# Kernel optimization log

Measured on AMD Instinct MI355X. Metric: run time of the kernel, lower is better.

The kernel has to match this reference:

```python
import jax, jax.numpy as jnp
import numpy as np

B, T, D = 8, 128, 1024   # batch, seq, n_embd
V, R, H = 4096, 16, 2    # vocab_size, rank, horizon


def setup_inputs() -> dict:
    key = jax.random.key(0)
    k1, k2, k3 = jax.random.split(key, 3)
    # scale 0.02 keeps exp(logits) numerically tame (pre-exp std ~ 0.6)
    last_hidden_state = jax.random.normal(k1, (B, T, D), jnp.float32) * 0.02
    param_w = jax.random.normal(k2, (V * R * H, D), jnp.float32) * 0.02
    param_b = jnp.zeros((V * R * H,), jnp.float32)
    points = jax.random.randint(k3, (B, H), 0, V, dtype=jnp.int64)
    return {
        "last_hidden_state": last_hidden_state,
        "param_w": param_w,
        "param_b": param_b,
        "points": points,
    }


def reference(last_hidden_state, param_w, param_b, points):
    # Take last timestep: (B, D)
    h_last = last_hidden_state[:, -1, :]
    # Linear + exp positivity: (B, H*V*R)
    params = jnp.exp(h_last @ param_w.T + param_b)
    # reshape to (B, H, V, R) matching torch .reshape(-1, horizon, vocab, rank)
    a = params.reshape(B, H, V, R)
    # CP outer product over rank: p_tilde[b,i,j] = sum_r a[b,0,i,r] * a[b,1,j,r]
    p_tilde = jnp.einsum('bir,bjr->bij', a[:, 0], a[:, 1])  # (B, V, V)
    # evaluate_at_points: gather p_tilde[b, points[b,0], points[b,1]]
    p_eval = p_tilde[jnp.arange(B), points[:, 0], points[:, 1]]  # (B,)
    # get_norm_const: sum over both vocab dims
    norm_const = p_tilde.sum(axis=(1, 2))  # (B,)
    return p_eval, norm_const
```

## Files before the change

### kernel.cpp

```cpp
#include <hip/hip_runtime.h>
#include <math.h>


#define B_ 8
#define T_ 128
#define D_ 1024
#define V_ 4096
#define R_ 16
#define H_ 2

__global__ void init_ws_kernel(float* ws) {
    int i = threadIdx.x;
    if (i < 512) ws[i] = 0.0f;
}

__device__ __forceinline__ float folded_reduce8(const float* p, int lane) {
    float t[4];
    {
        const bool hi = lane & 1;
#pragma unroll
        for (int i = 0; i < 4; ++i) {
            float send = hi ? p[i] : p[i + 4];
            float recv = __shfl_xor(send, 1);
            float keep = hi ? p[i + 4] : p[i];
            t[i] = keep + recv;
        }
    }
    float u[2];
    {
        const bool hi = lane & 2;
#pragma unroll
        for (int i = 0; i < 2; ++i) {
            float send = hi ? t[i] : t[i + 2];
            float recv = __shfl_xor(send, 2);
            float keep = hi ? t[i + 2] : t[i];
            u[i] = keep + recv;
        }
    }
    float wv;
    {
        const bool hi = lane & 4;
        float send = hi ? u[0] : u[1];
        float recv = __shfl_xor(send, 4);
        float keep = hi ? u[1] : u[0];
        wv = keep + recv;
    }
    wv += __shfl_xor(wv, 8);
    wv += __shfl_xor(wv, 16);
    wv += __shfl_xor(wv, 32);
    return wv;
}

__global__ __launch_bounds__(64, 2) void cpdist_main(
    const float* __restrict__ hid,
    const float* __restrict__ W,
    const float* __restrict__ bias,
    const int*   __restrict__ points,
    float* __restrict__ ws)
{
    const int lane = threadIdx.x;
    const int blk  = blockIdx.x;
    const int pair = blk >> 6;
    const int h    = pair >> 4;
    const int r    = pair & 15;
    const int v0   = (blk & 63) << 6;

    const int myb = ((lane & 1) << 2) | (lane & 2) | ((lane >> 2) & 1);

    float4 hreg[8][4];
#pragma unroll
    for (int b = 0; b < 8; ++b) {
        const float* hb = hid + ((size_t)b * T_ + (T_ - 1)) * D_;
#pragma unroll
        for (int j = 0; j < 4; ++j)
            hreg[b][j] = *reinterpret_cast<const float4*>(hb + j * 256 + lane * 4);
    }

    const int pv = points[myb * H_ + h];

    const size_t rowStride = (size_t)R_ * D_;
    const size_t row0 = ((size_t)h * V_ + v0) * R_ + r;
    const float* wp = W + row0 * D_;
    const float* bp = bias + row0;

    float4 cur[8];
#pragma unroll
    for (int j = 0; j < 4; ++j) {
        cur[j]     = *reinterpret_cast<const float4*>(wp + j * 256 + lane * 4);
        cur[4 + j] = *reinterpret_cast<const float4*>(wp + rowStride + j * 256 + lane * 4);
    }

    float accS = 0.0f;
    const int eidx = 256 + (myb * H_ + h) * R_ + r;

    for (int it = 0; it < 64; it += 2) {
        float4 nxt[8];
        if (it < 62) {
            const float* wn = wp + 2 * rowStride;
#pragma unroll
            for (int j = 0; j < 4; ++j) {
                nxt[j]     = *reinterpret_cast<const float4*>(wn + j * 256 + lane * 4);
                nxt[4 + j] = *reinterpret_cast<const float4*>(wn + rowStride + j * 256 + lane * 4);
            }
        }

        const float biasA = bp[(size_t)it * R_];
        const float biasB = bp[(size_t)(it + 1) * R_];

        float p[8];
#pragma unroll
        for (int b = 0; b < 8; ++b) {
            float s = 0.0f;
#pragma unroll
            for (int j = 0; j < 4; ++j) {
                s = fmaf(cur[j].x, hreg[b][j].x, s);
                s = fmaf(cur[j].y, hreg[b][j].y, s);
                s = fmaf(cur[j].z, hreg[b][j].z, s);
                s = fmaf(cur[j].w, hreg[b][j].w, s);
            }
            p[b] = s;
        }
        const float wvA = folded_reduce8(p, lane);

#pragma unroll
        for (int b = 0; b < 8; ++b) {
            float s = 0.0f;
#pragma unroll
            for (int j = 0; j < 4; ++j) {
                s = fmaf(cur[4 + j].x, hreg[b][j].x, s);
                s = fmaf(cur[4 + j].y, hreg[b][j].y, s);
                s = fmaf(cur[4 + j].z, hreg[b][j].z, s);
                s = fmaf(cur[4 + j].w, hreg[b][j].w, s);
            }
            p[b] = s;
        }
        const float wvB = folded_reduce8(p, lane);

        const float valA = __expf(wvA + biasA);
        const float valB = __expf(wvB + biasB);
        accS += valA;
        accS += valB;

        if (lane < 8) {
            if (v0 + it == pv)     ws[eidx] = valA;
            if (v0 + it + 1 == pv) ws[eidx] = valB;
        }

        if (it < 62) {
#pragma unroll
            for (int j = 0; j < 8; ++j) cur[j] = nxt[j];
            wp += 2 * rowStride;
        }
    }

    if (lane < 8)
        atomicAdd(&ws[(myb * H_ + h) * R_ + r], accS);
}

__global__ void cpdist_finalize(const float* __restrict__ ws, float* __restrict__ out) {
    const int tid = threadIdx.x;
    const int b = tid >> 4;
    const int r = tid & 15;
    const float e0 = ws[256 + (b * 2 + 0) * 16 + r];
    const float e1 = ws[256 + (b * 2 + 1) * 16 + r];
    const float s0 = ws[(b * 2 + 0) * 16 + r];
    const float s1 = ws[(b * 2 + 1) * 16 + r];
    float pe = e0 * e1;
    float nc = s0 * s1;
#pragma unroll
    for (int m = 1; m < 16; m <<= 1) {
        pe += __shfl_xor(pe, m);
        nc += __shfl_xor(nc, m);
    }
    if (r == 0) {
        out[b] = pe;
        out[8 + b] = nc;
    }
}

extern "C" void kernel_launch(void* const* d_in, const int* in_sizes, int n_in,
                              void* d_out, int out_size, void* d_ws, size_t ws_size,
                              hipStream_t stream) {
    const float* hid    = (const float*)d_in[0];
    const float* W      = (const float*)d_in[1];
    const float* bias   = (const float*)d_in[2];
    const int*   points = (const int*)d_in[3];
    float* out = (float*)d_out;
    float* ws  = (float*)d_ws;

    hipLaunchKernelGGL(init_ws_kernel, dim3(1), dim3(512), 0, stream, ws);
    hipLaunchKernelGGL(cpdist_main, dim3(2048), dim3(64), 0, stream,
                       hid, W, bias, points, ws);
    hipLaunchKernelGGL(cpdist_finalize, dim3(1), dim3(128), 0, stream, ws, out);
}
```

Before: 680.7 us.

## Replace atomic accumulation with per-block partial sums and stagger weight prefetch

Each block now writes its partial exp-sum to a dedicated workspace slot, and the finalize kernel reduces those partials. This removes the init kernel launch and the atomicAdd contention. The weight prefetch is also split so the next A rows load right after A is consumed and the next B rows load right after B is consumed, which replaces the full double buffer with a smaller staggered one and lowers register pressure. The finalize kernel does more serial work per thread, and the point-evaluation slots still rely on being written exactly once without being zeroed.

Result: no change. 671.7 us (-1.3%).

```diff
diff --git a/kernel.cpp b/kernel.cpp
--- a/kernel.cpp
+++ b/kernel.cpp
@@ -8,11 +8,6 @@
 #define V_ 4096
 #define R_ 16
 #define H_ 2
-
-__global__ void init_ws_kernel(float* ws) {
-    int i = threadIdx.x;
-    if (i < 512) ws[i] = 0.0f;
-}
 
 __device__ __forceinline__ float folded_reduce8(const float* p, int lane) {
     float t[4];
@@ -63,7 +58,8 @@
     const int pair = blk >> 6;
     const int h    = pair >> 4;
     const int r    = pair & 15;
-    const int v0   = (blk & 63) << 6;
+    const int vblk = blk & 63;
+    const int v0   = vblk << 6;
 
     const int myb = ((lane & 1) << 2) | (lane & 2) | ((lane >> 2) & 1);
 
@@ -83,27 +79,17 @@
     const float* wp = W + row0 * D_;
     const float* bp = bias + row0;
 
-    float4 cur[8];
+    float4 A[4], Bf[4];
 #pragma unroll
     for (int j = 0; j < 4; ++j) {
-        cur[j]     = *reinterpret_cast<const float4*>(wp + j * 256 + lane * 4);
-        cur[4 + j] = *reinterpret_cast<const float4*>(wp + rowStride + j * 256 + lane * 4);
+        A[j]  = *reinterpret_cast<const float4*>(wp + j * 256 + lane * 4);
+        Bf[j] = *reinterpret_cast<const float4*>(wp + rowStride + j * 256 + lane * 4);
     }
 
     float accS = 0.0f;
-    const int eidx = 256 + (myb * H_ + h) * R_ + r;
+    const int eidx = 16384 + (myb * H_ + h) * R_ + r;
 
     for (int it = 0; it < 64; it += 2) {
-        float4 nxt[8];
-        if (it < 62) {
-            const float* wn = wp + 2 * rowStride;
-#pragma unroll
-            for (int j = 0; j < 4; ++j) {
-                nxt[j]     = *reinterpret_cast<const float4*>(wn + j * 256 + lane * 4);
-                nxt[4 + j] = *reinterpret_cast<const float4*>(wn + rowStride + j * 256 + lane * 4);
-            }
-        }
-
         const float biasA = bp[(size_t)it * R_];
         const float biasB = bp[(size_t)(it + 1) * R_];
 
@@ -113,28 +99,42 @@
             float s = 0.0f;
 #pragma unroll
             for (int j = 0; j < 4; ++j) {
-                s = fmaf(cur[j].x, hreg[b][j].x, s);
-                s = fmaf(cur[j].y, hreg[b][j].y, s);
-                s = fmaf(cur[j].z, hreg[b][j].z, s);
-                s = fmaf(cur[j].w, hreg[b][j].w, s);
+                s = fmaf(A[j].x, hreg[b][j].x, s);
+                s = fmaf(A[j].y, hreg[b][j].y, s);
+                s = fmaf(A[j].z, hreg[b][j].z, s);
+                s = fmaf(A[j].w, hreg[b][j].w, s);
             }
             p[b] = s;
         }
         const float wvA = folded_reduce8(p, lane);
+
+        if (it < 62) {
+            const float* wn = wp + (size_t)(it + 2) * rowStride;
+#pragma unroll
+            for (int j = 0; j < 4; ++j)
+                A[j] = *reinterpret_cast<const float4*>(wn + j * 256 + lane * 4);
+        }
 
 #pragma unroll
         for (int b = 0; b < 8; ++b) {
             float s = 0.0f;
 #pragma unroll
             for (int j = 0; j < 4; ++j) {
-                s = fmaf(cur[4 + j].x, hreg[b][j].x, s);
-                s = fmaf(cur[4 + j].y, hreg[b][j].y, s);
-                s = fmaf(cur[4 + j].z, hreg[b][j].z, s);
-                s = fmaf(cur[4 + j].w, hreg[b][j].w, s);
+                s = fmaf(Bf[j].x, hreg[b][j].x, s);
+                s = fmaf(Bf[j].y, hreg[b][j].y, s);
+                s = fmaf(Bf[j].z, hreg[b][j].z, s);
+                s = fmaf(Bf[j].w, hreg[b][j].w, s);
             }
             p[b] = s;
         }
         const float wvB = folded_reduce8(p, lane);
+
+        if (it < 62) {
+            const float* wn = wp + (size_t)(it + 3) * rowStride;
+#pragma unroll
+            for (int j = 0; j < 4; ++j)
+                Bf[j] = *reinterpret_cast<const float4*>(wn + j * 256 + lane * 4);
+        }
 
         const float valA = __expf(wvA + biasA);
         const float valB = __expf(wvB + biasB);
@@ -145,34 +145,38 @@
             if (v0 + it == pv)     ws[eidx] = valA;
             if (v0 + it + 1 == pv) ws[eidx] = valB;
         }
-
-        if (it < 62) {
-#pragma unroll
-            for (int j = 0; j < 8; ++j) cur[j] = nxt[j];
-            wp += 2 * rowStride;
-        }
     }
 
     if (lane < 8)
-        atomicAdd(&ws[(myb * H_ + h) * R_ + r], accS);
+        ws[myb * 2048 + pair * 64 + vblk] = accS;
 }
 
 __global__ void cpdist_finalize(const float* __restrict__ ws, float* __restrict__ out) {
-    const int tid = threadIdx.x;
-    const int b = tid >> 4;
-    const int r = tid & 15;
-    const float e0 = ws[256 + (b * 2 + 0) * 16 + r];
-    const float e1 = ws[256 + (b * 2 + 1) * 16 + r];
-    const float s0 = ws[(b * 2 + 0) * 16 + r];
-    const float s1 = ws[(b * 2 + 1) * 16 + r];
-    float pe = e0 * e1;
-    float nc = s0 * s1;
+    const int t = threadIdx.x;
+    const int b = t >> 5;
+    const int h = (t >> 4) & 1;
+    const int r = t & 15;
+    const int pair = h * 16 + r;
+
+    const float* sp = ws + b * 2048 + pair * 64;
+    float S = 0.0f;
+#pragma unroll
+    for (int i = 0; i < 16; ++i) {
+        const float4 v4 = *reinterpret_cast<const float4*>(sp + i * 4);
+        S += v4.x + v4.y + v4.z + v4.w;
+    }
+    const float E = ws[16384 + (b * 2 + h) * 16 + r];
+
+    const float So = __shfl_xor(S, 16);
+    const float Eo = __shfl_xor(E, 16);
+    float nc = S * So;
+    float pe = E * Eo;
 #pragma unroll
     for (int m = 1; m < 16; m <<= 1) {
+        nc += __shfl_xor(nc, m);
         pe += __shfl_xor(pe, m);
-        nc += __shfl_xor(nc, m);
     }
-    if (r == 0) {
+    if ((t & 31) == 0) {
         out[b] = pe;
         out[8 + b] = nc;
     }
@@ -188,8 +192,7 @@
     float* out = (float*)d_out;
     float* ws  = (float*)d_ws;
 
-    hipLaunchKernelGGL(init_ws_kernel, dim3(1), dim3(512), 0, stream, ws);
     hipLaunchKernelGGL(cpdist_main, dim3(2048), dim3(64), 0, stream,
                        hid, W, bias, points, ws);
-    hipLaunchKernelGGL(cpdist_finalize, dim3(1), dim3(128), 0, stream, ws, out);
+    hipLaunchKernelGGL(cpdist_finalize, dim3(1), dim3(256), 0, stream, ws, out);
 }
```
